# Kernel optimization log

Hardware: AMD Instinct MI355X
Metric: run time of the kernel (lower is better)

## Reference

```python
import jax, jax.numpy as jnp
import numpy as np
from jax import lax

IN, H, L, NC = 1024, 256, 3, 8
B, T = 64, 512


def setup_inputs() -> dict:
    key = jax.random.key(0)
    ks = iter(jax.random.split(key, 32))
    def u(shape, fan_in):
        s = 1.0 / np.sqrt(fan_in)
        return jax.random.uniform(next(ks), shape, jnp.float32, -s, s)
    inp = {"x": jax.random.normal(next(ks), (B, T, IN), jnp.float32)}
    dims = [IN, H, H]
    for l in range(L):
        inp[f"Wih{l}"] = u((4 * H, dims[l]), H)
        inp[f"Whh{l}"] = u((4 * H, H), H)
        # combined bias b_ih + b_hh (mathematically identical)
        inp[f"b{l}"] = u((4 * H,), H) + u((4 * H,), H)
    inp["W1"] = u((128, H), H)
    inp["bfc1"] = u((128,), H)
    inp["W2"] = u((NC, 128), 128)
    inp["bfc2"] = u((NC,), 128)
    return inp


def _lstm_layer(x_tbd, Wih, Whh, b):
    # x_tbd: (T, B, D). Precompute input gates with one big GEMM.
    xg = jnp.einsum("tbd,gd->tbg", x_tbd, Wih) + b  # (T, B, 4H)
    h0 = jnp.zeros((x_tbd.shape[1], H), x_tbd.dtype)
    def step(carry, xg_t):
        h, c = carry
        g = xg_t + h @ Whh.T
        i, f, gg, o = jnp.split(g, 4, axis=-1)  # torch gate order i,f,g,o
        i, f, o = jax.nn.sigmoid(i), jax.nn.sigmoid(f), jax.nn.sigmoid(o)
        c = f * c + i * jnp.tanh(gg)
        h = o * jnp.tanh(c)
        return (h, c), h
    _, hs = lax.scan(step, (h0, h0), xg)
    return hs  # (T, B, H)


def reference(x, Wih0, Whh0, b0, Wih1, Whh1, b1, Wih2, Whh2, b2, W1, bfc1, W2, bfc2):
    h = jnp.transpose(x, (1, 0, 2))  # (T, B, IN)
    for Wih, Whh, b in ((Wih0, Whh0, b0), (Wih1, Whh1, b1), (Wih2, Whh2, b2)):
        h = _lstm_layer(h, Wih, Whh, b)
    last = h[-1]  # (B, H) output at final timestep
    z = jax.nn.relu(last @ W1.T + bfc1)
    return z @ W2.T + bfc2  # (B, NC)
```

## Files before the change

kernel.cpp:

```cpp
#include <hip/hip_runtime.h>
#include <hip/hip_cooperative_groups.h>
#include <cmath>

namespace cg = cooperative_groups;

#define IN_DIM 1024
#define HD 256
#define G4H 1024
#define BB 64
#define TT 512
#define NCLS 8

#define SLOT_STRIDE (HD * BB)
#define LAYER_STRIDE (4 * SLOT_STRIDE)

__device__ __forceinline__ float sigmoidf_(float x) {
    return 1.0f / (1.0f + __expf(-x));
}
__device__ __forceinline__ float tanhf_(float x) {
    return 2.0f / (1.0f + __expf(-2.0f * x)) - 1.0f;
}
__device__ __forceinline__ unsigned long long ld_agent_u64(const unsigned long long* p) {
    return __hip_atomic_load(p, __ATOMIC_RELAXED, __HIP_MEMORY_SCOPE_AGENT);
}
__device__ __forceinline__ void st_agent_u64(unsigned long long* p, unsigned long long v) {
    __hip_atomic_store(p, v, __ATOMIC_RELAXED, __HIP_MEMORY_SCOPE_AGENT);
}

#define GBM 128
#define GBN 128
#define GBK 16

__global__ __launch_bounds__(256) void xg0_gemm(const float* __restrict__ x,
                                                const float* __restrict__ Wih0,
                                                const float* __restrict__ b0,
                                                float* __restrict__ xg0T) {
    __shared__ float As[GBK][GBM];
    __shared__ float Bs[GBK][GBN];
    const int m0 = blockIdx.y * GBM;
    const int n0 = blockIdx.x * GBN;
    const int tid = threadIdx.x;
    const int tx = tid & 15;
    const int ty = tid >> 4;
    const int lr = tid >> 1;
    const int lk = (tid & 1) * 8;
    const int am = m0 + lr;
    const size_t arow = (size_t)(am & 63) * TT + (am >> 6);
    float acc[8][8] = {};
    for (int k0 = 0; k0 < IN_DIM; k0 += GBK) {
        const float4 a0 = *(const float4*)&x[arow * IN_DIM + k0 + lk];
        const float4 a1 = *(const float4*)&x[arow * IN_DIM + k0 + lk + 4];
        const float4 w0 = *(const float4*)&Wih0[(size_t)(n0 + lr) * IN_DIM + k0 + lk];
        const float4 w1 = *(const float4*)&Wih0[(size_t)(n0 + lr) * IN_DIM + k0 + lk + 4];
        __syncthreads();
        As[lk + 0][lr] = a0.x; As[lk + 1][lr] = a0.y; As[lk + 2][lr] = a0.z; As[lk + 3][lr] = a0.w;
        As[lk + 4][lr] = a1.x; As[lk + 5][lr] = a1.y; As[lk + 6][lr] = a1.z; As[lk + 7][lr] = a1.w;
        Bs[lk + 0][lr] = w0.x; Bs[lk + 1][lr] = w0.y; Bs[lk + 2][lr] = w0.z; Bs[lk + 3][lr] = w0.w;
        Bs[lk + 4][lr] = w1.x; Bs[lk + 5][lr] = w1.y; Bs[lk + 6][lr] = w1.z; Bs[lk + 7][lr] = w1.w;
        __syncthreads();
#pragma unroll
        for (int k = 0; k < GBK; ++k) {
            const float4 av0 = *(const float4*)&As[k][ty * 8];
            const float4 av1 = *(const float4*)&As[k][ty * 8 + 4];
            const float4 bv0 = *(const float4*)&Bs[k][tx * 8];
            const float4 bv1 = *(const float4*)&Bs[k][tx * 8 + 4];
            const float am8[8] = {av0.x, av0.y, av0.z, av0.w, av1.x, av1.y, av1.z, av1.w};
            const float bn8[8] = {bv0.x, bv0.y, bv0.z, bv0.w, bv1.x, bv1.y, bv1.z, bv1.w};
#pragma unroll
            for (int i = 0; i < 8; ++i)
#pragma unroll
                for (int jj = 0; jj < 8; ++jj)
                    acc[i][jj] = fmaf(am8[i], bn8[jj], acc[i][jj]);
        }
    }
    const float4 bias0 = *(const float4*)&b0[n0 + tx * 8];
    const float4 bias1 = *(const float4*)&b0[n0 + tx * 8 + 4];
    const float bia[8] = {bias0.x, bias0.y, bias0.z, bias0.w, bias1.x, bias1.y, bias1.z, bias1.w};
#pragma unroll
    for (int i = 0; i < 8; ++i) {
        const int m = m0 + ty * 8 + i;
        const int t = m >> 6;
        const int bb = m & 63;
#pragma unroll
        for (int jj = 0; jj < 8; ++jj) {
            const int n = n0 + tx * 8 + jj;
            xg0T[((size_t)t * G4H + n) * BB + bb] = acc[i][jj] + bia[jj];
        }
    }
}

__global__ __launch_bounds__(512) void lstm_cells(
    const float* __restrict__ xg0T,
    const float* __restrict__ Whh0,
    const float* __restrict__ Wih1, const float* __restrict__ Whh1, const float* __restrict__ b1,
    const float* __restrict__ Wih2, const float* __restrict__ Whh2, const float* __restrict__ b2,
    unsigned long long* __restrict__ ringU, int* __restrict__ flags)
{
    cg::grid_group grid = cg::this_grid();
    const int blk = blockIdx.x;
    const int layer = blk >> 6;
    const int lb = blk & 63;
    const int jbase = lb * 4;
    const int tid = threadIdx.x;
    const int w = tid >> 6;
    const int b = tid & 63;
    const int kbase = w * 32;

    __shared__ float red[2][16][8][64];

    const float* Wih = (layer == 1) ? Wih1 : Wih2;
    const float* Whh = (layer == 0) ? Whh0 : ((layer == 1) ? Whh1 : Whh2);
    const float* bias = (layer == 1) ? b1 : b2;

    float whreg[8];
    float wihreg[8];
    {
        const int r = b >> 2;
        const int jl = r >> 2;
        const int g = r & 3;
        const int kofs = kbase + (b & 3) * 8;
        const float4 h0 = *(const float4*)&Whh[(size_t)(g * HD + jbase + jl) * HD + kofs];
        const float4 h1 = *(const float4*)&Whh[(size_t)(g * HD + jbase + jl) * HD + kofs + 4];
        whreg[0] = h0.x; whreg[1] = h0.y; whreg[2] = h0.z; whreg[3] = h0.w;
        whreg[4] = h1.x; whreg[5] = h1.y; whreg[6] = h1.z; whreg[7] = h1.w;
        if (layer > 0) {
            const float4 i0 = *(const float4*)&Wih[(size_t)(g * HD + jbase + jl) * HD + kofs];
            const float4 i1 = *(const float4*)&Wih[(size_t)(g * HD + jbase + jl) * HD + kofs + 4];
            wihreg[0] = i0.x; wihreg[1] = i0.y; wihreg[2] = i0.z; wihreg[3] = i0.w;
            wihreg[4] = i1.x; wihreg[5] = i1.y; wihreg[6] = i1.z; wihreg[7] = i1.w;
        } else {
#pragma unroll
            for (int u = 0; u < 8; ++u) wihreg[u] = 0.0f;
        }
    }

    for (int i = blk * 512 + tid; i < 3 * LAYER_STRIDE; i += 192 * 512) ringU[i] = 0ull;
    for (int i = blk * 512 + tid; i < 3 * TT * 64; i += 192 * 512) flags[i] = 0;

    float bs0 = 0.f, bs1 = 0.f, bs2 = 0.f, bs3 = 0.f;
    if (layer > 0 && tid < 256) {
        bs0 = bias[0 * HD + jbase + w]; bs1 = bias[1 * HD + jbase + w];
        bs2 = bias[2 * HD + jbase + w]; bs3 = bias[3 * HD + jbase + w];
    }

    unsigned long long* myU = ringU + (size_t)layer * LAYER_STRIDE;
    const unsigned long long* inU = ringU + (size_t)(layer - 1) * LAYER_STRIDE;

    float c = 0.0f;

    grid.sync();

    for (int t = 0; t < TT; ++t) {
        const int p = t & 1;

        float xv0, xv1, xv2, xv3;
        if (layer == 0 && tid < 256) {
            const float* xg = xg0T + ((size_t)t * G4H + jbase + w) * BB + b;
            xv0 = xg[0 * HD * BB]; xv1 = xg[1 * HD * BB];
            xv2 = xg[2 * HD * BB]; xv3 = xg[3 * HD * BB];
        }
        __atomic_signal_fence(__ATOMIC_SEQ_CST);

        if (layer < 2 && t >= 4 && tid < 64) {
            const int* f_nxt = &flags[((layer + 1) * TT + (t - 4)) * 64 + tid];
            for (;;) {
                int ok = __hip_atomic_load(f_nxt, __ATOMIC_RELAXED, __HIP_MEMORY_SCOPE_AGENT);
                if (__all(ok)) break;
                __builtin_amdgcn_s_sleep(2);
            }
        }

        const unsigned long long* hp = myU + (size_t)((t + 3) & 3) * SLOT_STRIDE
                                     + (size_t)kbase * BB + b;
        unsigned long long v[32];
#pragma unroll
        for (int u = 0; u < 32; ++u) v[u] = ld_agent_u64(hp + (size_t)u * BB);
        __atomic_signal_fence(__ATOMIC_SEQ_CST);

        float acc[16];

        if (layer > 0) {
            const unsigned long long* gp = inU + (size_t)(t & 3) * SLOT_STRIDE
                                         + (size_t)kbase * BB + b;
            const unsigned wantg = (unsigned)(t + 1);
            unsigned long long v2[32];
            for (;;) {
#pragma unroll
                for (int u = 0; u < 32; ++u) v2[u] = ld_agent_u64(gp + (size_t)u * BB);
                unsigned ok = 1;
#pragma unroll
                for (int u = 0; u < 32; ++u) ok &= ((unsigned)(v2[u] >> 32) == wantg) ? 1u : 0u;
                if (__all(ok != 0)) break;
                __builtin_amdgcn_s_sleep(2);
            }
            float gv[32];
#pragma unroll
            for (int u = 0; u < 32; ++u) gv[u] = __uint_as_float((unsigned)v2[u]);
#pragma unroll
            for (int r = 0; r < 16; ++r) {
                float a = 0.0f;
#pragma unroll
                for (int q = 0; q < 4; ++q) {
#pragma unroll
                    for (int u = 0; u < 8; ++u) {
                        const float ws = __uint_as_float(
                            __builtin_amdgcn_readlane(__float_as_uint(wihreg[u]), r * 4 + q));
                        a = fmaf(ws, gv[q * 8 + u], a);
                    }
                }
                acc[r] = a;
            }
        } else {
#pragma unroll
            for (int r = 0; r < 16; ++r) acc[r] = 0.0f;
        }

        __atomic_signal_fence(__ATOMIC_SEQ_CST);

        {
            const unsigned want = (unsigned)t;
            for (;;) {
                unsigned ok = 1;
#pragma unroll
                for (int u = 0; u < 32; ++u) ok &= ((unsigned)(v[u] >> 32) == want) ? 1u : 0u;
                if (__all(ok != 0)) break;
                __builtin_amdgcn_s_sleep(2);
#pragma unroll
                for (int u = 0; u < 32; ++u) v[u] = ld_agent_u64(hp + (size_t)u * BB);
            }
        }
        float hv[32];
#pragma unroll
        for (int u = 0; u < 32; ++u) hv[u] = __uint_as_float((unsigned)v[u]);
#pragma unroll
        for (int r = 0; r < 16; ++r) {
            float a = acc[r];
#pragma unroll
            for (int q = 0; q < 4; ++q) {
#pragma unroll
                for (int u = 0; u < 8; ++u) {
                    const float ws = __uint_as_float(
                        __builtin_amdgcn_readlane(__float_as_uint(whreg[u]), r * 4 + q));
                    a = fmaf(ws, hv[q * 8 + u], a);
                }
            }
            acc[r] = a;
        }

#pragma unroll
        for (int r = 0; r < 16; ++r) red[p][r][w][b] = acc[r];
        __syncthreads();

        if (tid == 0) {
            __hip_atomic_store(&flags[(layer * TT + t) * 64 + lb], 1,
                               __ATOMIC_RELAXED, __HIP_MEMORY_SCOPE_AGENT);
        }

        if (tid < 256) {
            float a0, a1, a2, a3;
            if (layer == 0) { a0 = xv0; a1 = xv1; a2 = xv2; a3 = xv3; }
            else            { a0 = bs0; a1 = bs1; a2 = bs2; a3 = bs3; }
#pragma unroll
            for (int ww = 0; ww < 8; ++ww) {
                a0 += red[p][w * 4 + 0][ww][b];
                a1 += red[p][w * 4 + 1][ww][b];
                a2 += red[p][w * 4 + 2][ww][b];
                a3 += red[p][w * 4 + 3][ww][b];
            }
            const float ig = sigmoidf_(a0);
            const float fg = sigmoidf_(a1);
            const float gg = tanhf_(a2);
            const float og = sigmoidf_(a3);
            c = fg * c + ig * gg;
            const float h = og * tanhf_(c);
            const unsigned long long pk =
                ((unsigned long long)(unsigned)(t + 1) << 32) |
                (unsigned long long)__float_as_uint(h);
            st_agent_u64(&myU[(size_t)(t & 3) * SLOT_STRIDE
                              + (size_t)(jbase + w) * BB + b], pk);
        }
    }
}

__global__ __launch_bounds__(256) void classifier_k(
    const unsigned long long* __restrict__ ringU,
    const float* __restrict__ W1, const float* __restrict__ bfc1,
    const float* __restrict__ W2, const float* __restrict__ bfc2,
    float* __restrict__ out)
{
    __shared__ float z[BB * 128];
    const unsigned long long* h2T = ringU + 2 * LAYER_STRIDE
                                  + (size_t)((TT - 1) & 3) * SLOT_STRIDE;
    const int tid = threadIdx.x;
    for (int idx = tid; idx < BB * 128; idx += 256) {
        const int bb = idx >> 7;
        const int n = idx & 127;
        float acc = bfc1[n];
        const float* wr = W1 + (size_t)n * HD;
        for (int k = 0; k < HD; ++k) {
            const float hval = __uint_as_float((unsigned)h2T[(size_t)k * BB + bb]);
            acc = fmaf(hval, wr[k], acc);
        }
        z[bb * 128 + n] = fmaxf(acc, 0.0f);
    }
    __syncthreads();
    for (int idx = tid; idx < BB * NCLS; idx += 256) {
        const int bb = idx >> 3;
        const int n = idx & 7;
        float acc = bfc2[n];
        const float* zr = &z[bb * 128];
        const float* wr = W2 + (size_t)n * 128;
        for (int k = 0; k < 128; k += 4) {
            const float4 zv = *(const float4*)&zr[k];
            const float4 wv = *(const float4*)&wr[k];
            acc = fmaf(zv.x, wv.x, acc); acc = fmaf(zv.y, wv.y, acc);
            acc = fmaf(zv.z, wv.z, acc); acc = fmaf(zv.w, wv.w, acc);
        }
        out[idx] = acc;
    }
}

extern "C" void kernel_launch(void* const* d_in, const int* in_sizes, int n_in,
                              void* d_out, int out_size, void* d_ws, size_t ws_size,
                              hipStream_t stream) {
    const float* x    = (const float*)d_in[0];
    const float* Wih0 = (const float*)d_in[1];
    const float* Whh0 = (const float*)d_in[2];
    const float* b0   = (const float*)d_in[3];
    const float* Wih1 = (const float*)d_in[4];
    const float* Whh1 = (const float*)d_in[5];
    const float* b1   = (const float*)d_in[6];
    const float* Wih2 = (const float*)d_in[7];
    const float* Whh2 = (const float*)d_in[8];
    const float* b2   = (const float*)d_in[9];
    const float* W1   = (const float*)d_in[10];
    const float* bfc1 = (const float*)d_in[11];
    const float* W2   = (const float*)d_in[12];
    const float* bfc2 = (const float*)d_in[13];

    float* xg0T = (float*)d_ws;
    unsigned long long* ringU =
        (unsigned long long*)(xg0T + (size_t)BB * TT * G4H);
    int* flags = (int*)(ringU + 3 * LAYER_STRIDE);

    xg0_gemm<<<dim3(G4H / GBN, (BB * TT) / GBM), 256, 0, stream>>>(x, Wih0, b0, xg0T);

    const float* xgc = xg0T;
    unsigned long long* ru = ringU;
    int* fl = flags;
    void* args[] = {
        (void*)&xgc, (void*)&Whh0,
        (void*)&Wih1, (void*)&Whh1, (void*)&b1,
        (void*)&Wih2, (void*)&Whh2, (void*)&b2,
        (void*)&ru, (void*)&fl
    };
    hipLaunchCooperativeKernel((void*)lstm_cells, dim3(192), dim3(512), args, 0, stream);

    classifier_k<<<1, 256, 0, stream>>>(ringU, W1, bfc1, W2, bfc2, (float*)d_out);
}
```

Before: 7.099 ms.

## Software-pipeline the next step's input projection behind the gate update

Moves the loading of layer-0 precomputed gates, the wait on the next layer's flags, and the layer>0 input-to-hidden projection (Wih·h_{l-1}) for step t+1 to the end of step t, after the h store. This takes the input projection off the critical path between receiving h_{t-1} and computing the recurrent product. The first step is handled in a prologue before the loop. The h polling loop is restructured to poll with a shorter sleep. The extra preacc registers raise register pressure, and the order of the flag wait relative to the work has changed, so the ring protocol's safety margins need rechecking.

```diff
diff --git a/kernel.cpp b/kernel.cpp
--- a/kernel.cpp
+++ b/kernel.cpp
@@ -147,94 +147,77 @@
     const unsigned long long* inU = ringU + (size_t)(layer - 1) * LAYER_STRIDE;
 
     float c = 0.0f;
+    float preacc[16];
+    float xv0 = 0.f, xv1 = 0.f, xv2 = 0.f, xv3 = 0.f;
 
     grid.sync();
+
+    if (layer == 0) {
+        if (tid < 256) {
+            const float* xg = xg0T + ((size_t)0 * G4H + jbase + w) * BB + b;
+            xv0 = xg[0 * HD * BB]; xv1 = xg[1 * HD * BB];
+            xv2 = xg[2 * HD * BB]; xv3 = xg[3 * HD * BB];
+        }
+#pragma unroll
+        for (int r = 0; r < 16; ++r) preacc[r] = 0.0f;
+    } else {
+        const unsigned long long* gp = inU + (size_t)0 * SLOT_STRIDE
+                                     + (size_t)kbase * BB + b;
+        unsigned long long v2[32];
+        for (;;) {
+#pragma unroll
+            for (int u = 0; u < 32; ++u) v2[u] = ld_agent_u64(gp + (size_t)u * BB);
+            unsigned ok = 1;
+#pragma unroll
+            for (int u = 0; u < 32; ++u) ok &= ((unsigned)(v2[u] >> 32) == 1u) ? 1u : 0u;
+            if (__all(ok != 0)) break;
+            __builtin_amdgcn_s_sleep(2);
+        }
+        float gv[32];
+#pragma unroll
+        for (int u = 0; u < 32; ++u) gv[u] = __uint_as_float((unsigned)v2[u]);
+#pragma unroll
+        for (int r = 0; r < 16; ++r) {
+            float a = 0.0f;
+#pragma unroll
+            for (int q = 0; q < 4; ++q) {
+#pragma unroll
+                for (int u = 0; u < 8; ++u) {
+                    const float ws = __uint_as_float(
+                        __builtin_amdgcn_readlane(__float_as_uint(wihreg[u]), r * 4 + q));
+                    a = fmaf(ws, gv[q * 8 + u], a);
+                }
+            }
+            preacc[r] = a;
+        }
+    }
 
     for (int t = 0; t < TT; ++t) {
         const int p = t & 1;
 
-        float xv0, xv1, xv2, xv3;
-        if (layer == 0 && tid < 256) {
-            const float* xg = xg0T + ((size_t)t * G4H + jbase + w) * BB + b;
-            xv0 = xg[0 * HD * BB]; xv1 = xg[1 * HD * BB];
-            xv2 = xg[2 * HD * BB]; xv3 = xg[3 * HD * BB];
-        }
-        __atomic_signal_fence(__ATOMIC_SEQ_CST);
-
-        if (layer < 2 && t >= 4 && tid < 64) {
-            const int* f_nxt = &flags[((layer + 1) * TT + (t - 4)) * 64 + tid];
+
+        float hv[32];
+        {
+            const unsigned long long* hp = myU + (size_t)((t + 3) & 3) * SLOT_STRIDE
+                                         + (size_t)kbase * BB + b;
+            const unsigned want = (unsigned)t;
+            unsigned long long v[32];
             for (;;) {
-                int ok = __hip_atomic_load(f_nxt, __ATOMIC_RELAXED, __HIP_MEMORY_SCOPE_AGENT);
-                if (__all(ok)) break;
-                __builtin_amdgcn_s_sleep(2);
-            }
-        }
-
-        const unsigned long long* hp = myU + (size_t)((t + 3) & 3) * SLOT_STRIDE
-                                     + (size_t)kbase * BB + b;
-        unsigned long long v[32];
-#pragma unroll
-        for (int u = 0; u < 32; ++u) v[u] = ld_agent_u64(hp + (size_t)u * BB);
-        __atomic_signal_fence(__ATOMIC_SEQ_CST);
-
-        float acc[16];
-
-        if (layer > 0) {
-            const unsigned long long* gp = inU + (size_t)(t & 3) * SLOT_STRIDE
-                                         + (size_t)kbase * BB + b;
-            const unsigned wantg = (unsigned)(t + 1);
-            unsigned long long v2[32];
-            for (;;) {
-#pragma unroll
-                for (int u = 0; u < 32; ++u) v2[u] = ld_agent_u64(gp + (size_t)u * BB);
-                unsigned ok = 1;
-#pragma unroll
-                for (int u = 0; u < 32; ++u) ok &= ((unsigned)(v2[u] >> 32) == wantg) ? 1u : 0u;
-                if (__all(ok != 0)) break;
-                __builtin_amdgcn_s_sleep(2);
-            }
-            float gv[32];
-#pragma unroll
-            for (int u = 0; u < 32; ++u) gv[u] = __uint_as_float((unsigned)v2[u]);
-#pragma unroll
-            for (int r = 0; r < 16; ++r) {
-                float a = 0.0f;
-#pragma unroll
-                for (int q = 0; q < 4; ++q) {
-#pragma unroll
-                    for (int u = 0; u < 8; ++u) {
-                        const float ws = __uint_as_float(
-                            __builtin_amdgcn_readlane(__float_as_uint(wihreg[u]), r * 4 + q));
-                        a = fmaf(ws, gv[q * 8 + u], a);
-                    }
-                }
-                acc[r] = a;
-            }
-        } else {
-#pragma unroll
-            for (int r = 0; r < 16; ++r) acc[r] = 0.0f;
-        }
-
-        __atomic_signal_fence(__ATOMIC_SEQ_CST);
-
-        {
-            const unsigned want = (unsigned)t;
-            for (;;) {
+#pragma unroll
+                for (int u = 0; u < 32; ++u) v[u] = ld_agent_u64(hp + (size_t)u * BB);
                 unsigned ok = 1;
 #pragma unroll
                 for (int u = 0; u < 32; ++u) ok &= ((unsigned)(v[u] >> 32) == want) ? 1u : 0u;
                 if (__all(ok != 0)) break;
-                __builtin_amdgcn_s_sleep(2);
-#pragma unroll
-                for (int u = 0; u < 32; ++u) v[u] = ld_agent_u64(hp + (size_t)u * BB);
-            }
-        }
-        float hv[32];
-#pragma unroll
-        for (int u = 0; u < 32; ++u) hv[u] = __uint_as_float((unsigned)v[u]);
+                __builtin_amdgcn_s_sleep(1);
+            }
+#pragma unroll
+            for (int u = 0; u < 32; ++u) hv[u] = __uint_as_float((unsigned)v[u]);
+        }
+
 #pragma unroll
         for (int r = 0; r < 16; ++r) {
-            float a = acc[r];
+            float a = preacc[r];
 #pragma unroll
             for (int q = 0; q < 4; ++q) {
 #pragma unroll
@@ -244,11 +227,11 @@
                     a = fmaf(ws, hv[q * 8 + u], a);
                 }
             }
-            acc[r] = a;
-        }
-
-#pragma unroll
-        for (int r = 0; r < 16; ++r) red[p][r][w][b] = acc[r];
+            preacc[r] = a;
+        }
+
+#pragma unroll
+        for (int r = 0; r < 16; ++r) red[p][r][w][b] = preacc[r];
         __syncthreads();
 
         if (tid == 0) {
@@ -278,6 +261,58 @@
                 (unsigned long long)__float_as_uint(h);
             st_agent_u64(&myU[(size_t)(t & 3) * SLOT_STRIDE
                               + (size_t)(jbase + w) * BB + b], pk);
+        }
+
+        if (t + 1 < TT) {
+            if (layer < 2 && t + 1 >= 4 && tid < 64) {
+                const int* f_nxt = &flags[((layer + 1) * TT + (t - 3)) * 64 + tid];
+                for (;;) {
+                    int ok = __hip_atomic_load(f_nxt, __ATOMIC_RELAXED, __HIP_MEMORY_SCOPE_AGENT);
+                    if (__all(ok)) break;
+                    __builtin_amdgcn_s_sleep(2);
+                }
+            }
+
+            if (layer == 0) {
+                if (tid < 256) {
+                    const float* xg = xg0T + ((size_t)(t + 1) * G4H + jbase + w) * BB + b;
+                    xv0 = xg[0 * HD * BB]; xv1 = xg[1 * HD * BB];
+                    xv2 = xg[2 * HD * BB]; xv3 = xg[3 * HD * BB];
+                }
+#pragma unroll
+                for (int r = 0; r < 16; ++r) preacc[r] = 0.0f;
+            } else {
+                const unsigned long long* gp = inU + (size_t)((t + 1) & 3) * SLOT_STRIDE
+                                             + (size_t)kbase * BB + b;
+                const unsigned wantg = (unsigned)(t + 2);
+                unsigned long long v2[32];
+                for (;;) {
+#pragma unroll
+                    for (int u = 0; u < 32; ++u) v2[u] = ld_agent_u64(gp + (size_t)u * BB);
+                    unsigned ok = 1;
+#pragma unroll
+                    for (int u = 0; u < 32; ++u) ok &= ((unsigned)(v2[u] >> 32) == wantg) ? 1u : 0u;
+                    if (__all(ok != 0)) break;
+                    __builtin_amdgcn_s_sleep(2);
+                }
+                float gv[32];
+#pragma unroll
+                for (int u = 0; u < 32; ++u) gv[u] = __uint_as_float((unsigned)v2[u]);
+#pragma unroll
+                for (int r = 0; r < 16; ++r) {
+                    float a = 0.0f;
+#pragma unroll
+                    for (int q = 0; q < 4; ++q) {
+#pragma unroll
+                        for (int u = 0; u < 8; ++u) {
+                            const float ws = __uint_as_float(
+                                __builtin_amdgcn_readlane(__float_as_uint(wihreg[u]), r * 4 + q));
+                            a = fmaf(ws, gv[q * 8 + u], a);
+                        }
+                    }
+                    preacc[r] = a;
+                }
+            }
         }
     }
 }
```

Result: faster. 6.092 ms (-14.2%).
